# Kernel optimization log

Measured on AMD Instinct MI355X. Metric: run time of the kernel, lower is better.

Reference implementation:

```python
import jax, jax.numpy as jnp
import numpy as np

LATENT = 128
HEADS = 4
HEAD_DIM = LATENT // HEADS
NUM_BUCKETS = 32
MAX_DISTANCE = 100000
B, N = 8, 2048


def relative_position_bucket(qpos, kpos):
    """T5-style bidirectional relative position bucketing.
    qpos, kpos: [B, N] int -> buckets [B, N, N] int32 in [0, NUM_BUCKETS).
    """
    rel = kpos[:, None, :] - qpos[:, :, None]  # [B, Nq, Nk]
    half = NUM_BUCKETS // 2
    buckets = (rel > 0).astype(jnp.int32) * half
    arel = jnp.abs(rel)
    max_exact = half // 2
    is_small = arel < max_exact
    # log-spaced buckets for larger distances
    large = max_exact + (
        jnp.log(jnp.maximum(arel, 1).astype(jnp.float32) / max_exact)
        / np.log(MAX_DISTANCE / max_exact)
        * (half - max_exact)
    ).astype(jnp.int32)
    large = jnp.minimum(large, half - 1)
    return buckets + jnp.where(is_small, arel.astype(jnp.int32), large)


def setup_inputs() -> dict:
    key = jax.random.key(0)
    ks = jax.random.split(key, 12)
    s = 0.02
    x = jax.random.normal(ks[0], (B, N, LATENT), dtype=jnp.float32)
    positions = jnp.sort(jax.random.randint(ks[1], (B, N), 0, 1000000), axis=-1)
    mask = jnp.ones((B, N), dtype=bool)
    Wq = jax.random.normal(ks[2], (LATENT, LATENT), dtype=jnp.float32) * s
    bq = jax.random.normal(ks[3], (LATENT,), dtype=jnp.float32) * s
    Wk = jax.random.normal(ks[4], (LATENT, LATENT), dtype=jnp.float32) * s
    bk = jax.random.normal(ks[5], (LATENT,), dtype=jnp.float32) * s
    Wv = jax.random.normal(ks[6], (LATENT, LATENT), dtype=jnp.float32) * s
    bv = jax.random.normal(ks[7], (LATENT,), dtype=jnp.float32) * s
    pos_w = jax.random.normal(ks[8], (NUM_BUCKETS + 1, HEADS), dtype=jnp.float32) * s
    Wo = jax.random.normal(ks[9], (LATENT, LATENT), dtype=jnp.float32) * s
    bo = jax.random.normal(ks[10], (LATENT,), dtype=jnp.float32) * s
    return {"x": x, "positions": positions, "mask": mask,
            "Wq": Wq, "bq": bq, "Wk": Wk, "bk": bk, "Wv": Wv, "bv": bv,
            "pos_w": pos_w, "Wo": Wo, "bo": bo}


def reference(x, positions, mask, Wq, bq, Wk, bk, Wv, bv, pos_w, Wo, bo):
    b, n, _ = x.shape
    # QKV projections, split heads: [b, h, n, d]
    Q = (x @ Wq + bq).reshape(b, n, HEADS, HEAD_DIM).transpose(0, 2, 1, 3)
    K = (x @ Wk + bk).reshape(b, n, HEADS, HEAD_DIM).transpose(0, 2, 1, 3)
    V = (x @ Wv + bv).reshape(b, n, HEADS, HEAD_DIM).transpose(0, 2, 1, 3)
    scores = jnp.einsum("bhqd,bhkd->bhqk", Q, K) / jnp.sqrt(
        jnp.asarray(HEAD_DIM, dtype=x.dtype))
    buckets = relative_position_bucket(positions, positions)  # [b, n, n]
    bias = pos_w[buckets]                  # [b, n, n, h]
    scores = scores + bias.transpose(0, 3, 1, 2)  # [b, h, n, n]
    scores = jnp.where(mask[:, None, None, :], scores, -jnp.inf)
    attn = jax.nn.softmax(scores, axis=-1)
    attn = jnp.nan_to_num(attn, nan=0.0)
    attended = jnp.einsum("bhqk,bhkd->bhqd", attn, V)
    attended = attended.transpose(0, 2, 1, 3).reshape(b, n, LATENT)
    return attended @ Wo + bo
```

## Files before the change

### kernel.cpp

```cpp
#include <hip/hip_runtime.h>
#include <math.h>


#define LOG2E 1.4426950408889634f
#define QKV_SCALE 0.17677669529663687f
#define QS (QKV_SCALE * LOG2E)

typedef _Float16 half8 __attribute__((ext_vector_type(8)));
typedef float ffrag __attribute__((ext_vector_type(4)));

#if __has_builtin(__builtin_amdgcn_exp2f)
#define EXP2F __builtin_amdgcn_exp2f
#else
#define EXP2F exp2f
#endif

static __device__ __forceinline__ unsigned short f16bits(float f) {
    return __builtin_bit_cast(unsigned short, (_Float16)f);
}
static __device__ __forceinline__ float h16f(unsigned int bits) {
    return (float)__builtin_bit_cast(_Float16, (unsigned short)(bits & 0xFFFFu));
}
static __device__ __forceinline__ unsigned int pk2(float a, float b) {
    return __builtin_bit_cast(unsigned int, __builtin_amdgcn_cvt_pkrtz(a, b));
}
static __device__ __forceinline__ void async_cp16(const unsigned short* g, unsigned short* l) {
    __builtin_amdgcn_global_load_lds(
        (const __attribute__((address_space(1))) unsigned int*)g,
        (__attribute__((address_space(3))) unsigned int*)l, 16, 0, 0);
}

__device__ __constant__ int SN_TAB[32] = {
     -2000000000,
    -30755, -9458, -2908, -894, -275, -84, -26,
    -7, -6, -5, -4, -3, -2, -1,
    0,
    1, 2, 3, 4, 5, 6, 7,
    8,
    27, 85, 276, 895, 2909, 9459, 30756,
    2000000000 };

__global__ __launch_bounds__(256)
void prep_seg_kernel(const float* __restrict__ Wq, const float* __restrict__ Wk,
                     const float* __restrict__ Wv, const float* __restrict__ Wo,
                     const float* __restrict__ bq, const float* __restrict__ bk,
                     const float* __restrict__ bv,
                     const int* __restrict__ positions,
                     unsigned short* __restrict__ Wt_qkv,
                     unsigned short* __restrict__ Wt_o,
                     float* __restrict__ bias_qkv,
                     unsigned int* __restrict__ segtab)
{
    if (blockIdx.x < 256) {
        const int e = blockIdx.x * 256 + threadIdx.x;
        const int m = e >> 14, r = e & 16383;
        const int c = r >> 7, k = r & 127;
        float v;
        if (m == 0)      v = Wq[k * 128 + c] * QS;
        else if (m == 1) v = Wk[k * 128 + c];
        else if (m == 2) v = Wv[k * 128 + c];
        else             v = Wo[k * 128 + c];
        if (m < 3) Wt_qkv[(m * 128 + c) * 128 + k] = f16bits(v);
        else       Wt_o[c * 128 + k] = f16bits(v);
        if (e < 128)      bias_qkv[e] = bq[e] * QS;
        else if (e < 256) bias_qkv[e] = bk[e - 128];
        else if (e < 384) bias_qkv[e] = bv[e - 256];
        return;
    }
    const int gid = (blockIdx.x - 256) * 256 + threadIdx.x;
    const int row = gid >> 5;
    const int s = gid & 31;
    const int b = row >> 11;
    const int* kp = positions + b * 2048;
    const int qp = kp[row & 2047];
    const int bucket = (s < 15) ? (15 - s) : (s == 15 ? 0 : s + 1);
    if (s == 31) { segtab[row * 32 + s] = (2048u << 16) | 31u; return; }
    const int target = qp + SN_TAB[s + 1];
    int lo = 0, hi = 2048;
    while (lo < hi) { const int mid = (lo + hi) >> 1; if (kp[mid] < target) lo = mid + 1; else hi = mid; }
    segtab[row * 32 + s] = ((unsigned)lo << 16) | (unsigned)bucket;
}

__global__ __launch_bounds__(512)
void qkv_mfma(const float* __restrict__ x, const unsigned short* __restrict__ Wt,
              const float* __restrict__ bias_qkv,
              unsigned short* __restrict__ Qb, unsigned short* __restrict__ Kb,
              unsigned short* __restrict__ Vg2)
{
    __shared__ __align__(16) unsigned short Xs[64 * 136];
    const int tid = threadIdx.x;
    const int token0 = blockIdx.x * 64;
    #pragma unroll
    for (int it = 0; it < 4; ++it) {
        const int f = tid + it * 512;
        const int row = f >> 5, k0 = (f & 31) << 2;
        const float4 xv = *(const float4*)(x + (size_t)(token0 + row) * 128 + k0);
        uint2 u;
        u.x = pk2(xv.x, xv.y);
        u.y = pk2(xv.z, xv.w);
        *(uint2*)(Xs + row * 136 + k0) = u;
    }
    __syncthreads();

    const int wave = tid >> 6, lane = tid & 63;
    const int lq = lane & 15, quad = lane >> 4;
    const int b = token0 >> 11;
    const int n0 = token0 & 2047;

    #pragma unroll
    for (int j = 0; j < 3; ++j) {
        const int ct = wave + j * 8;
        const int colbase = ct * 16;
        half8 wf[4];
        #pragma unroll
        for (int ks = 0; ks < 4; ++ks)
            wf[ks] = *(const half8*)(Wt + (colbase + lq) * 128 + ks * 32 + quad * 8);

        if (ct < 16) {
            const int c0q = colbase + quad * 4;
            const float4 bv = *(const float4*)(bias_qkv + c0q);
            #pragma unroll
            for (int msub = 0; msub < 4; ++msub) {
                ffrag acc = {bv.x, bv.y, bv.z, bv.w};
                #pragma unroll
                for (int ks = 0; ks < 4; ++ks) {
                    const half8 xf = *(const half8*)(Xs + (msub * 16 + lq) * 136 + ks * 32 + quad * 8);
                    acc = __builtin_amdgcn_mfma_f32_16x16x32_f16(wf[ks], xf, acc, 0, 0, 0);
                }
                const int n = n0 + msub * 16 + lq;
                const int c0 = c0q & 127;
                const int h = c0 >> 5, d = c0 & 31;
                const ushort4 v4 = make_ushort4(f16bits(acc[0]), f16bits(acc[1]),
                                                f16bits(acc[2]), f16bits(acc[3]));
                unsigned short* base = (ct < 8) ? Qb : Kb;
                *(ushort4*)(base + ((size_t)(b * 4 + h) * 2048 + n) * 32 + d) = v4;
            }
        } else {
            const float bias = bias_qkv[colbase + lq];
            const int c2 = colbase + lq - 256;
            const int h = c2 >> 5, d = c2 & 31;
            const size_t bhh = (size_t)(b * 4 + h);
            #pragma unroll
            for (int msub = 0; msub < 4; ++msub) {
                ffrag acc = {bias, bias, bias, bias};
                #pragma unroll
                for (int ks = 0; ks < 4; ++ks) {
                    const half8 xf = *(const half8*)(Xs + (msub * 16 + lq) * 136 + ks * 32 + quad * 8);
                    acc = __builtin_amdgcn_mfma_f32_16x16x32_f16(xf, wf[ks], acc, 0, 0, 0);
                }
                const int n = n0 + msub * 16 + quad * 4;
                const int chunk = n >> 6;
                const int kloc = n & 63;
                const int win = kloc >> 5;
                const int halfq = (kloc >> 4) & 1;
                const int slot = d * 8 + (((win << 2) | quad) ^ (d & 7));
                const size_t off = (((size_t)bhh * 32 + chunk) * 256 + slot) * 8 + halfq * 4;
                const ushort4 v4 = make_ushort4(f16bits(acc[0]), f16bits(acc[1]),
                                                f16bits(acc[2]), f16bits(acc[3]));
                *(ushort4*)(Vg2 + off) = v4;
            }
        }
    }
}

__global__ __launch_bounds__(512, 6)
void attn_kernel(const unsigned short* __restrict__ Qb,
                 const unsigned short* __restrict__ Kb,
                 const unsigned short* __restrict__ Vg2,
                 const unsigned int* __restrict__ segtab,
                 const float* __restrict__ pos_w,
                 unsigned short* __restrict__ att)
{
    __shared__ __align__(16) unsigned short VB[4][2][2048];
    __shared__ unsigned int Sg[32 * 32];

    const int tid = threadIdx.x;
    const int wave = __builtin_amdgcn_readfirstlane(tid >> 6);
    const int lane = tid & 63;
    const int lq = lane & 15, quad = lane >> 4;
    const int group = wave >> 1, wg = wave & 1;

    const int qt = blockIdx.x & 63;
    const int bh = blockIdx.x >> 6;
    const int b = bh >> 2, h = bh & 3;
    const int q0 = qt * 32;

    const unsigned short* Kg = Kb + (size_t)bh * 2048 * 32;
    const unsigned short* Vgb = Vg2 + (size_t)bh * 65536;

    #pragma unroll
    for (int it = 0; it < 2; ++it) {
        const int g = (wg * 2 + it) * 64 + lane;
        async_cp16(Vgb + (size_t)group * 2048 + g * 8, &VB[group][0][(wg * 2 + it) * 512]);
    }

    if (tid < 256) {
        const unsigned int* src = segtab + ((size_t)b * 2048 + q0) * 32;
        uint4 u = *(const uint4*)(src + tid * 4);
        unsigned int* c = &u.x;
        const int row = tid >> 3, s0 = (tid & 7) * 4;
        const int rx = row & 31;
        #pragma unroll
        for (int i = 0; i < 4; ++i) {
            const float wf = __expf(pos_w[(c[i] & 0xFFFFu) * 4 + h]);
            Sg[row * 32 + ((s0 + i) ^ rx)] = (c[i] & 0xFFFF0000u) | f16bits(wf);
        }
    }

    const int qa = q0 + wg * 16 + lq;
    const half8 qf = *(const half8*)(Qb + ((size_t)bh * 2048 + qa) * 32 + quad * 8);

    half8 ones;
    #pragma unroll
    for (int i = 0; i < 8; ++i) ones[i] = (_Float16)1.0f;

    ffrag o0 = {0.f,0.f,0.f,0.f}, o1 = {0.f,0.f,0.f,0.f}, o2 = {0.f,0.f,0.f,0.f};
    int cur = -1, endk = 0; float wfv = 0.f;
    const int rowa = wg * 16 + lq;
    const int sga = rowa * 32, xa = rowa & 31;

    const int koff = lq * 32 + quad * 8;

#define LDK(base) (*(const half8*)(Kg + (size_t)(base) * 32 + koff))

    half8 kP[2], kN[2];
    {
        const int kb0 = group * 64;
        kP[0] = LDK(kb0);
        kP[1] = LDK(kb0 + 16);
    }

    __syncthreads();

    auto do_half = [&](const half8* kf2, const unsigned short* vb, int kc, int dw) {
        unsigned int pu[4];
        #pragma unroll
        for (int T = 0; T < 2; ++T) {
            const half8 kf = kf2[T];
            ffrag s = {0.f,0.f,0.f,0.f};
            s = __builtin_amdgcn_mfma_f32_16x16x32_f16(kf, qf, s, 0, 0, 0);
            const int kidx = kc + (dw * 2 + T) * 16 + quad * 4;
            float p[4];
            if (__builtin_expect(__any(kidx + 3 >= endk), 0)) {
                #pragma unroll
                for (int r = 0; r < 4; ++r) {
                    while (kidx + r >= endk) {
                        const unsigned int u = Sg[sga + ((++cur) ^ xa)];
                        endk = (int)(u >> 16); wfv = h16f(u);
                    }
                    p[r] = EXP2F(s[r]) * wfv;
                }
            } else {
                #pragma unroll
                for (int r = 0; r < 4; ++r) p[r] = EXP2F(s[r]) * wfv;
            }
            pu[T * 2 + 0] = pk2(p[0], p[1]);
            pu[T * 2 + 1] = pk2(p[2], p[3]);
        }
        const int sl = ((dw << 2) | quad) ^ (lq & 7);
        const half8 A0 = *(const half8*)(vb + (lq * 8 + sl) * 8);
        const half8 A1 = *(const half8*)(vb + ((16 + lq) * 8 + sl) * 8);
        const half8 Bx = __builtin_bit_cast(half8, make_int4(pu[0], pu[1], pu[2], pu[3]));
        o0 = __builtin_amdgcn_mfma_f32_16x16x32_f16(A0, Bx, o0, 0, 0, 0);
        o1 = __builtin_amdgcn_mfma_f32_16x16x32_f16(A1, Bx, o1, 0, 0, 0);
        o2 = __builtin_amdgcn_mfma_f32_16x16x32_f16(ones, Bx, o2, 0, 0, 0);
    };

    for (int ii = 0; ii < 4; ++ii) {
        {
            const int kc = ii * 512 + group * 64;
            #pragma unroll
            for (int it = 0; it < 2; ++it) {
                const int g = (wg * 2 + it) * 64 + lane;
                async_cp16(Vgb + (size_t)((2 * ii + 1) * 4 + group) * 2048 + g * 8,
                           &VB[group][1][(wg * 2 + it) * 512]);
            }
            kN[0] = LDK(kc + 32);
            kN[1] = LDK(kc + 48);
            do_half(kP, &VB[group][0][0], kc, 0);
            kP[0] = LDK(kc + 256);
            kP[1] = LDK(kc + 272);
            do_half(kN, &VB[group][0][0], kc, 1);
            __syncthreads();
        }
        {
            const int kco = ii * 512 + group * 64 + 256;
            if (ii < 3) {
                #pragma unroll
                for (int it = 0; it < 2; ++it) {
                    const int g = (wg * 2 + it) * 64 + lane;
                    async_cp16(Vgb + (size_t)((2 * ii + 2) * 4 + group) * 2048 + g * 8,
                               &VB[group][0][(wg * 2 + it) * 512]);
                }
            }
            kN[0] = LDK(kco + 32);
            kN[1] = LDK(kco + 48);
            do_half(kP, &VB[group][1][0], kco, 0);
            const int kcn = (ii < 3) ? kco + 256 : kco;
            kP[0] = LDK(kcn);
            kP[1] = LDK(kcn + 16);
            do_half(kN, &VB[group][1][0], kco, 1);
            __syncthreads();
        }
    }
#undef LDK

    float ls = o2[0];
    float* scr = (float*)&VB[0][0][0];
    if (group != 0) {
        float* sp = scr + (((group - 1) * 2 + wg) * 64 + lane) * 9;
        #pragma unroll
        for (int j = 0; j < 4; ++j) { sp[j] = o0[j]; sp[4 + j] = o1[j]; }
        sp[8] = ls;
    }
    __syncthreads();
    if (group == 0) {
        #pragma unroll
        for (int g = 0; g < 3; ++g) {
            const float* sp = scr + ((g * 2 + wg) * 64 + lane) * 9;
            #pragma unroll
            for (int j = 0; j < 4; ++j) { o0[j] += sp[j]; o1[j] += sp[4 + j]; }
            ls += sp[8];
        }
        const float inv = 1.0f / ls;
        unsigned short* da = att + (size_t)(b * 2048 + qa) * 128 + h * 32 + quad * 4;
        uint2 r0, r1;
        r0.x = pk2(o0[0] * inv, o0[1] * inv);
        r0.y = pk2(o0[2] * inv, o0[3] * inv);
        r1.x = pk2(o1[0] * inv, o1[1] * inv);
        r1.y = pk2(o1[2] * inv, o1[3] * inv);
        *(uint2*)da = r0;
        *(uint2*)(da + 16) = r1;
    }
}

__global__ __launch_bounds__(512)
void out_mfma(const unsigned short* __restrict__ att,
              const unsigned short* __restrict__ Wt_o,
              const float* __restrict__ bo, float* __restrict__ out)
{
    __shared__ __align__(16) unsigned short Xs[64 * 136];
    const int tid = threadIdx.x;
    const int token0 = blockIdx.x * 64;
    #pragma unroll
    for (int it = 0; it < 2; ++it) {
        const int f = tid + it * 512;
        const int row = f >> 4, k0 = (f & 15) << 3;
        const uint4 v = *(const uint4*)(att + (size_t)(token0 + row) * 128 + k0);
        *(uint4*)(Xs + row * 136 + k0) = v;
    }
    __syncthreads();

    const int wave = tid >> 6, lane = tid & 63;
    const int lq = lane & 15, quad = lane >> 4;
    const int colbase = wave * 16;

    half8 wf[4];
    #pragma unroll
    for (int ks = 0; ks < 4; ++ks)
        wf[ks] = *(const half8*)(Wt_o + (colbase + lq) * 128 + ks * 32 + quad * 8);
    const float4 bv = *(const float4*)(bo + colbase + quad * 4);

    #pragma unroll
    for (int msub = 0; msub < 4; ++msub) {
        ffrag acc = {bv.x, bv.y, bv.z, bv.w};
        #pragma unroll
        for (int ks = 0; ks < 4; ++ks) {
            const half8 xf = *(const half8*)(Xs + (msub * 16 + lq) * 136 + ks * 32 + quad * 8);
            acc = __builtin_amdgcn_mfma_f32_16x16x32_f16(wf[ks], xf, acc, 0, 0, 0);
        }
        const int c0 = colbase + quad * 4;
        *(float4*)(out + (size_t)(token0 + msub * 16 + lq) * 128 + c0) =
            make_float4(acc[0], acc[1], acc[2], acc[3]);
    }
}

extern "C" void kernel_launch(void* const* d_in, const int* in_sizes, int n_in,
                              void* d_out, int out_size, void* d_ws, size_t ws_size,
                              hipStream_t stream)
{
    const float* x         = (const float*)d_in[0];
    const int*   positions = (const int*)d_in[1];
    const float* Wq = (const float*)d_in[3];
    const float* bq = (const float*)d_in[4];
    const float* Wk = (const float*)d_in[5];
    const float* bk = (const float*)d_in[6];
    const float* Wv = (const float*)d_in[7];
    const float* bv = (const float*)d_in[8];
    const float* pw = (const float*)d_in[9];
    const float* Wo = (const float*)d_in[10];
    const float* bo = (const float*)d_in[11];
    float* out = (float*)d_out;

    unsigned short* Qb  = (unsigned short*)d_ws;
    unsigned short* Kb  = Qb + 2097152;
    unsigned short* Vg2 = Kb + 2097152;
    unsigned short* att = Vg2 + 2097152;
    unsigned int* segtab = (unsigned int*)(att + 2097152);
    unsigned short* Wt_qkv = (unsigned short*)(segtab + 524288);
    unsigned short* Wt_o = Wt_qkv + 49152;
    float* bias_qkv = (float*)(Wt_o + 16384);

    prep_seg_kernel<<<2304, 256, 0, stream>>>(Wq, Wk, Wv, Wo, bq, bk, bv, positions,
                                              Wt_qkv, Wt_o, bias_qkv, segtab);
    qkv_mfma<<<256, 512, 0, stream>>>(x, Wt_qkv, bias_qkv, Qb, Kb, Vg2);
    attn_kernel<<<2048, 512, 0, stream>>>(Qb, Kb, Vg2, segtab, pw, att);
    out_mfma<<<256, 512, 0, stream>>>(att, Wt_o, bo, out);
}
```

Baseline: 161.2 us.

## Widen attention query tile to 64 rows and split keys across two wave groups

The attention kernel now gives each block 64 query rows (four waves per group) and splits keys between two groups instead of four, each handling 128-key chunks. The V layout from the QKV kernel is reorganised into 128-key chunks with a 16-way XOR swizzle to match. The block count halves, so each K/V tile loaded into shared memory serves twice as many queries, and the cross-group reduction at the end is smaller. In exchange it holds more K fragments in registers per wave, which can lower occupancy, and there are fewer blocks to spread across the GPU.

```diff
diff --git a/kernel.cpp b/kernel.cpp
--- a/kernel.cpp
+++ b/kernel.cpp
@@ -149,12 +149,11 @@
                     acc = __builtin_amdgcn_mfma_f32_16x16x32_f16(xf, wf[ks], acc, 0, 0, 0);
                 }
                 const int n = n0 + msub * 16 + quad * 4;
-                const int chunk = n >> 6;
-                const int kloc = n & 63;
-                const int win = kloc >> 5;
-                const int halfq = (kloc >> 4) & 1;
-                const int slot = d * 8 + (((win << 2) | quad) ^ (d & 7));
-                const size_t off = (((size_t)bhh * 32 + chunk) * 256 + slot) * 8 + halfq * 4;
+                const int chunk = n >> 7, kloc = n & 127;
+                const int win = kloc >> 5, rem = kloc & 31;
+                const int half = rem >> 4, pg = (rem >> 2) & 3;
+                const int G = d * 16 + ((win * 4 + pg) ^ (d & 15));
+                const size_t off = ((bhh * 16 + chunk) * 512 + G) * 8 + half * 4;
                 const ushort4 v4 = make_ushort4(f16bits(acc[0]), f16bits(acc[1]),
                                                 f16bits(acc[2]), f16bits(acc[3]));
                 *(ushort4*)(Vg2 + off) = v4;
@@ -171,19 +170,19 @@
                  const float* __restrict__ pos_w,
                  unsigned short* __restrict__ att)
 {
-    __shared__ __align__(16) unsigned short VB[4][2][2048];
-    __shared__ unsigned int Sg[32 * 32];
+    __shared__ __align__(16) unsigned short VB[2][2][4096];
+    __shared__ unsigned int Sg[64 * 32];
 
     const int tid = threadIdx.x;
     const int wave = __builtin_amdgcn_readfirstlane(tid >> 6);
     const int lane = tid & 63;
     const int lq = lane & 15, quad = lane >> 4;
-    const int group = wave >> 1, wg = wave & 1;
-
-    const int qt = blockIdx.x & 63;
-    const int bh = blockIdx.x >> 6;
+    const int group = wave >> 2, wg = wave & 3;
+
+    const int qt = blockIdx.x & 31;
+    const int bh = blockIdx.x >> 5;
     const int b = bh >> 2, h = bh & 3;
-    const int q0 = qt * 32;
+    const int q0 = qt * 64;
 
     const unsigned short* Kg = Kb + (size_t)bh * 2048 * 32;
     const unsigned short* Vgb = Vg2 + (size_t)bh * 65536;
@@ -191,10 +190,10 @@
     #pragma unroll
     for (int it = 0; it < 2; ++it) {
         const int g = (wg * 2 + it) * 64 + lane;
-        async_cp16(Vgb + (size_t)group * 2048 + g * 8, &VB[group][0][(wg * 2 + it) * 512]);
-    }
-
-    if (tid < 256) {
+        async_cp16(Vgb + (size_t)group * 4096 + g * 8, &VB[group][0][(wg * 2 + it) * 512]);
+    }
+
+    {
         const unsigned int* src = segtab + ((size_t)b * 2048 + q0) * 32;
         uint4 u = *(const uint4*)(src + tid * 4);
         unsigned int* c = &u.x;
@@ -219,109 +218,94 @@
     const int rowa = wg * 16 + lq;
     const int sga = rowa * 32, xa = rowa & 31;
 
-    const int koff = lq * 32 + quad * 8;
-
-#define LDK(base) (*(const half8*)(Kg + (size_t)(base) * 32 + koff))
-
-    half8 kP[2], kN[2];
+    half8 kA[4], kB[4];
     {
-        const int kb0 = group * 64;
-        kP[0] = LDK(kb0);
-        kP[1] = LDK(kb0 + 16);
+        const int kc0 = group * 128;
+        #pragma unroll
+        for (int j = 0; j < 4; ++j)
+            kA[j] = *(const half8*)(Kg + (size_t)(kc0 + j * 16 + lq) * 32 + quad * 8);
     }
 
     __syncthreads();
 
-    auto do_half = [&](const half8* kf2, const unsigned short* vb, int kc, int dw) {
-        unsigned int pu[4];
-        #pragma unroll
-        for (int T = 0; T < 2; ++T) {
-            const half8 kf = kf2[T];
-            ffrag s = {0.f,0.f,0.f,0.f};
-            s = __builtin_amdgcn_mfma_f32_16x16x32_f16(kf, qf, s, 0, 0, 0);
-            const int kidx = kc + (dw * 2 + T) * 16 + quad * 4;
-            float p[4];
-            if (__builtin_expect(__any(kidx + 3 >= endk), 0)) {
-                #pragma unroll
-                for (int r = 0; r < 4; ++r) {
-                    while (kidx + r >= endk) {
-                        const unsigned int u = Sg[sga + ((++cur) ^ xa)];
-                        endk = (int)(u >> 16); wfv = h16f(u);
+    auto half_chunk = [&](const half8* karr, const unsigned short* vb, int kc, int w0) {
+        #pragma unroll
+        for (int dw = 0; dw < 2; ++dw) {
+            const int w = w0 + dw;
+            unsigned int pu[4];
+            #pragma unroll
+            for (int T = 0; T < 2; ++T) {
+                const half8 kf = karr[dw * 2 + T];
+                ffrag s = {0.f,0.f,0.f,0.f};
+                s = __builtin_amdgcn_mfma_f32_16x16x32_f16(kf, qf, s, 0, 0, 0);
+                const int kidx = kc + (w * 2 + T) * 16 + quad * 4;
+                float p[4];
+                if (__builtin_expect(__any(kidx + 3 >= endk), 0)) {
+                    #pragma unroll
+                    for (int r = 0; r < 4; ++r) {
+                        while (kidx + r >= endk) {
+                            const unsigned int u = Sg[sga + ((++cur) ^ xa)];
+                            endk = (int)(u >> 16); wfv = h16f(u);
+                        }
+                        p[r] = EXP2F(s[r]) * wfv;
                     }
-                    p[r] = EXP2F(s[r]) * wfv;
+                } else {
+                    #pragma unroll
+                    for (int r = 0; r < 4; ++r) p[r] = EXP2F(s[r]) * wfv;
                 }
-            } else {
-                #pragma unroll
-                for (int r = 0; r < 4; ++r) p[r] = EXP2F(s[r]) * wfv;
+                pu[T * 2 + 0] = pk2(p[0], p[1]);
+                pu[T * 2 + 1] = pk2(p[2], p[3]);
             }
-            pu[T * 2 + 0] = pk2(p[0], p[1]);
-            pu[T * 2 + 1] = pk2(p[2], p[3]);
-        }
-        const int sl = ((dw << 2) | quad) ^ (lq & 7);
-        const half8 A0 = *(const half8*)(vb + (lq * 8 + sl) * 8);
-        const half8 A1 = *(const half8*)(vb + ((16 + lq) * 8 + sl) * 8);
-        const half8 Bx = __builtin_bit_cast(half8, make_int4(pu[0], pu[1], pu[2], pu[3]));
-        o0 = __builtin_amdgcn_mfma_f32_16x16x32_f16(A0, Bx, o0, 0, 0, 0);
-        o1 = __builtin_amdgcn_mfma_f32_16x16x32_f16(A1, Bx, o1, 0, 0, 0);
-        o2 = __builtin_amdgcn_mfma_f32_16x16x32_f16(ones, Bx, o2, 0, 0, 0);
+            const int c = (w * 4 + quad) ^ lq;
+            const half8 A0 = *(const half8*)(vb + (lq * 16 + c) * 8);
+            const half8 A1 = *(const half8*)(vb + ((16 + lq) * 16 + c) * 8);
+            const half8 Bx = __builtin_bit_cast(half8, make_int4(pu[0], pu[1], pu[2], pu[3]));
+            o0 = __builtin_amdgcn_mfma_f32_16x16x32_f16(A0, Bx, o0, 0, 0, 0);
+            o1 = __builtin_amdgcn_mfma_f32_16x16x32_f16(A1, Bx, o1, 0, 0, 0);
+            o2 = __builtin_amdgcn_mfma_f32_16x16x32_f16(ones, Bx, o2, 0, 0, 0);
+        }
     };
 
-    for (int ii = 0; ii < 4; ++ii) {
-        {
-            const int kc = ii * 512 + group * 64;
+    for (int i = 0; i < 8; ++i) {
+        const int kc = (2 * i + group) * 128;
+        const unsigned short* vb = &VB[group][i & 1][0];
+        if (i < 7) {
             #pragma unroll
             for (int it = 0; it < 2; ++it) {
                 const int g = (wg * 2 + it) * 64 + lane;
-                async_cp16(Vgb + (size_t)((2 * ii + 1) * 4 + group) * 2048 + g * 8,
-                           &VB[group][1][(wg * 2 + it) * 512]);
+                async_cp16(Vgb + (size_t)(2 * i + group + 2) * 4096 + g * 8,
+                           &VB[group][(i + 1) & 1][(wg * 2 + it) * 512]);
             }
-            kN[0] = LDK(kc + 32);
-            kN[1] = LDK(kc + 48);
-            do_half(kP, &VB[group][0][0], kc, 0);
-            kP[0] = LDK(kc + 256);
-            kP[1] = LDK(kc + 272);
-            do_half(kN, &VB[group][0][0], kc, 1);
-            __syncthreads();
-        }
-        {
-            const int kco = ii * 512 + group * 64 + 256;
-            if (ii < 3) {
-                #pragma unroll
-                for (int it = 0; it < 2; ++it) {
-                    const int g = (wg * 2 + it) * 64 + lane;
-                    async_cp16(Vgb + (size_t)((2 * ii + 2) * 4 + group) * 2048 + g * 8,
-                               &VB[group][0][(wg * 2 + it) * 512]);
-                }
-            }
-            kN[0] = LDK(kco + 32);
-            kN[1] = LDK(kco + 48);
-            do_half(kP, &VB[group][1][0], kco, 0);
-            const int kcn = (ii < 3) ? kco + 256 : kco;
-            kP[0] = LDK(kcn);
-            kP[1] = LDK(kcn + 16);
-            do_half(kN, &VB[group][1][0], kco, 1);
-            __syncthreads();
-        }
-    }
-#undef LDK
+        }
+        #pragma unroll
+        for (int j = 0; j < 4; ++j)
+            kB[j] = *(const half8*)(Kg + (size_t)(kc + (4 + j) * 16 + lq) * 32 + quad * 8);
+
+        half_chunk(kA, vb, kc, 0);
+
+        const int kcn = (i < 7) ? kc + 256 : kc;
+        #pragma unroll
+        for (int j = 0; j < 4; ++j)
+            kA[j] = *(const half8*)(Kg + (size_t)(kcn + j * 16 + lq) * 32 + quad * 8);
+
+        half_chunk(kB, vb, kc, 2);
+        __syncthreads();
+    }
 
     float ls = o2[0];
     float* scr = (float*)&VB[0][0][0];
-    if (group != 0) {
-        float* sp = scr + (((group - 1) * 2 + wg) * 64 + lane) * 9;
+    if (group == 1) {
+        float* sp = scr + (wg * 64 + lane) * 9;
         #pragma unroll
         for (int j = 0; j < 4; ++j) { sp[j] = o0[j]; sp[4 + j] = o1[j]; }
         sp[8] = ls;
     }
     __syncthreads();
     if (group == 0) {
-        #pragma unroll
-        for (int g = 0; g < 3; ++g) {
-            const float* sp = scr + ((g * 2 + wg) * 64 + lane) * 9;
-            #pragma unroll
-            for (int j = 0; j < 4; ++j) { o0[j] += sp[j]; o1[j] += sp[4 + j]; }
-            ls += sp[8];
-        }
+        const float* sp = scr + (wg * 64 + lane) * 9;
+        #pragma unroll
+        for (int j = 0; j < 4; ++j) { o0[j] += sp[j]; o1[j] += sp[4 + j]; }
+        ls += sp[8];
         const float inv = 1.0f / ls;
         unsigned short* da = att + (size_t)(b * 2048 + qa) * 128 + h * 32 + quad * 4;
         uint2 r0, r1;
@@ -404,6 +388,6 @@
     prep_seg_kernel<<<2304, 256, 0, stream>>>(Wq, Wk, Wv, Wo, bq, bk, bv, positions,
                                               Wt_qkv, Wt_o, bias_qkv, segtab);
     qkv_mfma<<<256, 512, 0, stream>>>(x, Wt_qkv, bias_qkv, Qb, Kb, Vg2);
-    attn_kernel<<<2048, 512, 0, stream>>>(Qb, Kb, Vg2, segtab, pw, att);
+    attn_kernel<<<1024, 512, 0, stream>>>(Qb, Kb, Vg2, segtab, pw, att);
     out_mfma<<<256, 512, 0, stream>>>(att, Wt_o, bo, out);
 }
```

New measurement: 165.2 us. 1.02x slower.
